# Performance work log

Measured on AMD Instinct MI355X. Metric: run time of the kernel, lower is better.

## Reference

```python
import jax, jax.numpy as jnp
import numpy as np

N_NODES = 50000
N_EDGES = 800000
IN_CH = 64
EDGE_DIM = 8
HIDDEN = 128
NUM_GRAPHS = 256


def setup_inputs() -> dict:
    key = jax.random.key(0)
    ks = jax.random.split(key, 16)
    x = jax.random.normal(ks[0], (N_NODES, IN_CH), dtype=jnp.float32)
    edge_index = jax.random.randint(ks[1], (2, N_EDGES), 0, N_NODES, dtype=jnp.int64)
    edge_attr = jax.random.normal(ks[2], (N_EDGES, EDGE_DIM), dtype=jnp.float32)
    batch = jnp.sort(jax.random.randint(ks[3], (N_NODES,), 0, NUM_GRAPHS, dtype=jnp.int64))

    def lin(k, fan_in, fan_out):
        bound = 1.0 / np.sqrt(fan_in)
        kw, kb = jax.random.split(k)
        W = jax.random.uniform(kw, (fan_in, fan_out), minval=-bound, maxval=bound, dtype=jnp.float32)
        b = jax.random.uniform(kb, (fan_out,), minval=-bound, maxval=bound, dtype=jnp.float32)
        return W, b

    W1, b1 = lin(ks[4], IN_CH, HIDDEN)
    We1, be1 = lin(ks[5], EDGE_DIM, IN_CH)
    W2, b2 = lin(ks[6], HIDDEN, HIDDEN)
    We2, be2 = lin(ks[7], EDGE_DIM, HIDDEN)
    W3, b3 = lin(ks[8], HIDDEN, HIDDEN)
    We3, be3 = lin(ks[9], EDGE_DIM, HIDDEN)
    return {"x": x, "edge_index": edge_index, "edge_attr": edge_attr, "batch": batch,
            "W1": W1, "b1": b1, "We1": We1, "be1": be1,
            "W2": W2, "b2": b2, "We2": We2, "be2": be2,
            "W3": W3, "b3": b3, "We3": We3, "be3": be3}


def gine_conv(x, src, dst, edge_attr, W, b, We, be):
    # edge feature projection to node-feature dim, then message = relu(x_j + e)
    e = edge_attr @ We + be                      # [E, d]
    msg = jax.nn.relu(x[src] + e)                # [E, d]
    agg = jax.ops.segment_sum(msg, dst, num_segments=x.shape[0])  # [N, d]
    # eps = 0 (PyG default, not trainable)
    return (x + agg) @ W + b


def reference(x, edge_index, edge_attr, batch,
              W1, b1, We1, be1, W2, b2, We2, be2, W3, b3, We3, be3):
    x = x.astype(jnp.float32)
    edge_attr = edge_attr.astype(jnp.float32)
    src, dst = edge_index[0], edge_index[1]
    x = jax.nn.relu(gine_conv(x, src, dst, edge_attr, W1, b1, We1, be1))
    x = jax.nn.relu(gine_conv(x, src, dst, edge_attr, W2, b2, We2, be2))
    x = jax.nn.relu(gine_conv(x, src, dst, edge_attr, W3, b3, We3, be3))
    # global mean pool over graphs
    sums = jax.ops.segment_sum(x, batch, num_segments=NUM_GRAPHS)          # [G, d]
    counts = jax.ops.segment_sum(jnp.ones((x.shape[0],), x.dtype), batch, num_segments=NUM_GRAPHS)
    return sums / jnp.maximum(counts, 1.0)[:, None]
```

## Files before the change

### kernel.cpp

```cpp
#include <hip/hip_runtime.h>
#include <hip/hip_bf16.h>
#include <hip/hip_fp16.h>

#define N_NODES 50000
#define N_EDGES 800000
#define IN_CH 64
#define EDGE_DIM 8
#define HIDDEN 128
#define NUM_GRAPHS 256
#define NPASS 2
#define PASS_W ((N_NODES + NPASS - 1) / NPASS)

typedef __attribute__((ext_vector_type(8))) _Float16 half8;
typedef __attribute__((ext_vector_type(4))) float floatx4;
typedef __attribute__((ext_vector_type(4))) int intx4;

static __device__ __forceinline__ __half2 u2h(int u) {
    union { int i; __half2 h; } cv; cv.i = u; return cv.h;
}
static __device__ __forceinline__ int h2u(__half2 h) {
    union { __half2 h; int i; } cv; cv.h = h; return cv.i;
}
static __device__ __forceinline__ unsigned short h1u(__half h) {
    union { __half h; unsigned short u; } cv; cv.h = h; return cv.u;
}

__global__ __launch_bounds__(256) void hist_kernel(
    const int* __restrict__ dst, int* __restrict__ deg, int E)
{
    int i = blockIdx.x * blockDim.x + threadIdx.x;
    if (i < E) atomicAdd(&deg[dst[i]], 1);
}

__global__ __launch_bounds__(256) void scan1_kernel(
    const int* __restrict__ deg, int* __restrict__ incl,
    int* __restrict__ blockSums, int N)
{
    __shared__ int s[256];
    int b = blockIdx.x, t = threadIdx.x;
    int i0 = b * 512 + 2 * t;
    int a0 = (i0 < N) ? deg[i0] : 0;
    int a1 = (i0 + 1 < N) ? deg[i0 + 1] : 0;
    int ps = a0 + a1;
    s[t] = ps;
    __syncthreads();
    for (int off = 1; off < 256; off <<= 1) {
        int v = (t >= off) ? s[t - off] : 0;
        __syncthreads();
        s[t] += v;
        __syncthreads();
    }
    int exclp = s[t] - ps;
    if (i0 < N)     incl[i0]     = exclp + a0;
    if (i0 + 1 < N) incl[i0 + 1] = exclp + a0 + a1;
    if (t == 255) blockSums[b] = s[255];
}

__global__ __launch_bounds__(128) void scan2_kernel(int* __restrict__ blockSums, int B)
{
    __shared__ int s[128];
    int t = threadIdx.x;
    int v = (t < B) ? blockSums[t] : 0;
    s[t] = v;
    __syncthreads();
    for (int off = 1; off < 128; off <<= 1) {
        int u = (t >= off) ? s[t - off] : 0;
        __syncthreads();
        s[t] += u;
        __syncthreads();
    }
    if (t < B) blockSums[t] = s[t] - v;
}

__global__ __launch_bounds__(256) void scan3_kernel(
    const int* __restrict__ incl, const int* __restrict__ deg,
    const int* __restrict__ blockSums, int* __restrict__ rowptr,
    int* __restrict__ pos, int N)
{
    int i = blockIdx.x * blockDim.x + threadIdx.x;
    if (i >= N) return;
    int v = incl[i] - deg[i] + blockSums[i >> 9];
    rowptr[i] = v;
    pos[i] = v;
}

__global__ __launch_bounds__(256) void scatter_pass_kernel(
    const int* __restrict__ dst, int* __restrict__ pos,
    int* __restrict__ eid, int lo, int E)
{
    int e = blockIdx.x * blockDim.x + threadIdx.x;
    if (e >= E) return;
    int d = dst[e];
    if ((unsigned)(d - lo) >= (unsigned)PASS_W) return;
    int p = atomicAdd(&pos[d], 1);
    eid[p] = e;
}

__global__ __launch_bounds__(256) void ranksort_gather_kernel(
    const int* __restrict__ eid, const int* __restrict__ src,
    const float* __restrict__ ea,
    const int* __restrict__ rowptr, const int* __restrict__ deg,
    int* __restrict__ src_s, __half* __restrict__ ea16, int N)
{
    int wave = threadIdx.x >> 6;
    int lane = threadIdx.x & 63;
    int n = blockIdx.x * 4 + wave;
    if (n >= N) return;
    int s = __builtin_amdgcn_readfirstlane(rowptr[n]);
    int d = __builtin_amdgcn_readfirstlane(deg[n]);

    if (d <= 64) {
        int e = (lane < d) ? eid[s + lane] : 0x7fffffff;
        int rank = 0;
        for (int i = 0; i < d; ++i) {
            int v = __builtin_amdgcn_readlane(e, i);
            rank += (v < e) ? 1 : 0;
        }
        if (lane < d) {
            int p = s + rank;
            src_s[p] = src[e];
            const float4* q = (const float4*)(ea + (size_t)e * EDGE_DIM);
            float4 a = q[0], b = q[1];
            __half2* o = (__half2*)(ea16 + (size_t)p * EDGE_DIM);
            o[0] = __floats2half2_rn(a.x, a.y);
            o[1] = __floats2half2_rn(a.z, a.w);
            o[2] = __floats2half2_rn(b.x, b.y);
            o[3] = __floats2half2_rn(b.z, b.w);
        }
    } else {
        for (int l = lane; l < d; l += 64) {
            int e = eid[s + l];
            int rank = 0;
            for (int i = 0; i < d; ++i)
                rank += (eid[s + i] < e) ? 1 : 0;
            int p = s + rank;
            src_s[p] = src[e];
            const float4* q = (const float4*)(ea + (size_t)e * EDGE_DIM);
            float4 a = q[0], b = q[1];
            __half2* o = (__half2*)(ea16 + (size_t)p * EDGE_DIM);
            o[0] = __floats2half2_rn(a.x, a.y);
            o[1] = __floats2half2_rn(a.z, a.w);
            o[2] = __floats2half2_rn(b.x, b.y);
            o[3] = __floats2half2_rn(b.z, b.w);
        }
    }
}

#define XH_ELEMS (N_NODES * IN_CH)
__global__ __launch_bounds__(256) void cvt_all_kernel(
    const float* __restrict__ x, __half* __restrict__ xh,
    const float* __restrict__ W1, const float* __restrict__ W2,
    const float* __restrict__ W3,
    _Float16* __restrict__ Wt1, _Float16* __restrict__ Wt2,
    _Float16* __restrict__ Wt3)
{
    int idx = blockIdx.x * blockDim.x + threadIdx.x;
    if (idx < XH_ELEMS) { xh[idx] = __float2half(x[idx]); return; }
    idx -= XH_ELEMS;
    if (idx < 128 * IN_CH) {
        int n = idx / IN_CH, k = idx - n * IN_CH;
        Wt1[idx] = (_Float16)W1[k * 128 + n];
        return;
    }
    idx -= 128 * IN_CH;
    if (idx < 128 * HIDDEN) {
        int n = idx / HIDDEN, k = idx - n * HIDDEN;
        Wt2[idx] = (_Float16)W2[k * 128 + n];
        return;
    }
    idx -= 128 * HIDDEN;
    if (idx < 128 * HIDDEN) {
        int n = idx / HIDDEN, k = idx - n * HIDDEN;
        Wt3[idx] = (_Float16)W3[k * 128 + n];
    }
}

#define BF 8

__global__ __launch_bounds__(256) void gather_xs128_kernel(
    const __half* __restrict__ h,
    const int*    __restrict__ src_s,
    const __half* __restrict__ ea16,
    const int*    __restrict__ rowptr,
    const int*    __restrict__ deg,
    const float*  __restrict__ We,
    const float*  __restrict__ be,
    __half*       __restrict__ xs,
    int N)
{
    int wave = threadIdx.x >> 6;
    int n    = blockIdx.x * 4 + wave;
    if (n >= N) return;
    int l  = threadIdx.x & 63;
    int j0 = 2 * l;

    __half2 hw[8];
    #pragma unroll
    for (int k = 0; k < 8; ++k) {
        float2 wv = *(const float2*)&We[k * 128 + j0];
        hw[k] = __floats2half2_rn(wv.x, wv.y);
    }
    float2 bevf = *(const float2*)&be[j0];
    __half2 bev2 = __floats2half2_rn(bevf.x, bevf.y);

    int start = __builtin_amdgcn_readfirstlane(rowptr[n]);
    int dg    = __builtin_amdgcn_readfirstlane(deg[n]);

    float2 hf = __half22float2(*(const __half2*)&h[(size_t)n * 128 + j0]);
    float acc0 = hf.x, acc1 = hf.y;

    int nb = dg / BF;
    int base = start;
    for (int b = 0; b < nb; ++b, base += BF) {
        int sid[BF];
        #pragma unroll
        for (int t = 0; t < BF; ++t)
            sid[t] = __builtin_amdgcn_readfirstlane(
                __builtin_nontemporal_load(&src_s[base + t]));
        __half2 hraw[BF];
        #pragma unroll
        for (int t = 0; t < BF; ++t)
            hraw[t] = *(const __half2*)&h[(size_t)sid[t] * 128 + j0];
        intx4 eav[BF];
        #pragma unroll
        for (int t = 0; t < BF; ++t)
            eav[t] = __builtin_nontemporal_load(
                (const intx4*)&ea16[(size_t)(base + t) * 8]);

        #pragma unroll
        for (int t = 0; t < BF; ++t) {
            __half2 e01 = u2h(eav[t].x), e23 = u2h(eav[t].y);
            __half2 e45 = u2h(eav[t].z), e67 = u2h(eav[t].w);
            __half2 m = __hfma2(__low2half2(e01),  hw[0], bev2);
            m = __hfma2(__high2half2(e01), hw[1], m);
            m = __hfma2(__low2half2(e23),  hw[2], m);
            m = __hfma2(__high2half2(e23), hw[3], m);
            m = __hfma2(__low2half2(e45),  hw[4], m);
            m = __hfma2(__high2half2(e45), hw[5], m);
            m = __hfma2(__low2half2(e67),  hw[6], m);
            m = __hfma2(__high2half2(e67), hw[7], m);
            m = __hadd2(m, hraw[t]);
            float2 mf = __half22float2(m);
            acc0 += mf.x > 0.0f ? mf.x : 0.0f;
            acc1 += mf.y > 0.0f ? mf.y : 0.0f;
        }
    }
    int end = start + dg;
    for (int idx = base; idx < end; ++idx) {
        int s = __builtin_amdgcn_readfirstlane(src_s[idx]);
        __half2 hr = *(const __half2*)&h[(size_t)s * 128 + j0];
        intx4 ev = __builtin_nontemporal_load((const intx4*)&ea16[(size_t)idx * 8]);
        __half2 e01 = u2h(ev.x), e23 = u2h(ev.y), e45 = u2h(ev.z), e67 = u2h(ev.w);
        __half2 m = __hfma2(__low2half2(e01),  hw[0], bev2);
        m = __hfma2(__high2half2(e01), hw[1], m);
        m = __hfma2(__low2half2(e23),  hw[2], m);
        m = __hfma2(__high2half2(e23), hw[3], m);
        m = __hfma2(__low2half2(e45),  hw[4], m);
        m = __hfma2(__high2half2(e45), hw[5], m);
        m = __hfma2(__low2half2(e67),  hw[6], m);
        m = __hfma2(__high2half2(e67), hw[7], m);
        m = __hadd2(m, hr);
        float2 mf = __half22float2(m);
        acc0 += mf.x > 0.0f ? mf.x : 0.0f;
        acc1 += mf.y > 0.0f ? mf.y : 0.0f;
    }
    __builtin_nontemporal_store(h2u(__floats2half2_rn(acc0, acc1)),
                                (int*)&xs[(size_t)n * 128 + j0]);
}

__global__ __launch_bounds__(256) void gather_xs64_kernel(
    const __half* __restrict__ h,
    const int*    __restrict__ src_s,
    const __half* __restrict__ ea16,
    const int*    __restrict__ rowptr,
    const int*    __restrict__ deg,
    const float*  __restrict__ We,
    const float*  __restrict__ be,
    __half*       __restrict__ xs,
    int N)
{
    int wave = threadIdx.x >> 6;
    int n    = blockIdx.x * 4 + wave;
    if (n >= N) return;
    int j = threadIdx.x & 63;

    __half2 w2[4];
    #pragma unroll
    for (int p = 0; p < 4; ++p)
        w2[p] = __floats2half2_rn(We[(2 * p) * 64 + j], We[(2 * p + 1) * 64 + j]);
    float bej = be[j];

    int start = __builtin_amdgcn_readfirstlane(rowptr[n]);
    int dg    = __builtin_amdgcn_readfirstlane(deg[n]);

    float acc = __half2float(h[(size_t)n * 64 + j]);

    int nb = dg / BF;
    int base = start;
    for (int b = 0; b < nb; ++b, base += BF) {
        int sid[BF];
        #pragma unroll
        for (int t = 0; t < BF; ++t)
            sid[t] = __builtin_amdgcn_readfirstlane(
                __builtin_nontemporal_load(&src_s[base + t]));
        __half hraw[BF];
        #pragma unroll
        for (int t = 0; t < BF; ++t)
            hraw[t] = h[(size_t)sid[t] * 64 + j];
        intx4 eav[BF];
        #pragma unroll
        for (int t = 0; t < BF; ++t)
            eav[t] = __builtin_nontemporal_load(
                (const intx4*)&ea16[(size_t)(base + t) * 8]);

        #pragma unroll
        for (int t = 0; t < BF; ++t) {
            __half2 d = __hmul2(u2h(eav[t].x), w2[0]);
            d = __hfma2(u2h(eav[t].y), w2[1], d);
            d = __hfma2(u2h(eav[t].z), w2[2], d);
            d = __hfma2(u2h(eav[t].w), w2[3], d);
            float proj = __half2float(__low2half(d)) + __half2float(__high2half(d));
            float m = __half2float(hraw[t]) + proj + bej;
            acc += m > 0.0f ? m : 0.0f;
        }
    }
    int end = start + dg;
    for (int idx = base; idx < end; ++idx) {
        int s = __builtin_amdgcn_readfirstlane(src_s[idx]);
        __half hr = h[(size_t)s * 64 + j];
        intx4 ev = __builtin_nontemporal_load((const intx4*)&ea16[(size_t)idx * 8]);
        __half2 d = __hmul2(u2h(ev.x), w2[0]);
        d = __hfma2(u2h(ev.y), w2[1], d);
        d = __hfma2(u2h(ev.z), w2[2], d);
        d = __hfma2(u2h(ev.w), w2[3], d);
        float proj = __half2float(__low2half(d)) + __half2float(__high2half(d));
        float m = __half2float(hr) + proj + bej;
        acc += m > 0.0f ? m : 0.0f;
    }
    __builtin_nontemporal_store(h1u(__float2half(acc)),
                                (unsigned short*)&xs[(size_t)n * 64 + j]);
}

template<int K>
__global__ __launch_bounds__(256) void node_mfma_kernel(
    const _Float16* __restrict__ xs,
    const _Float16* __restrict__ Wt,
    const float*    __restrict__ b,
    _Float16*       __restrict__ out,
    int N)
{
    int wave  = threadIdx.x >> 6;
    int lane  = threadIdx.x & 63;
    int row16 = lane & 15;
    int quad  = lane >> 4;
    int m0    = (blockIdx.x * 4 + wave) * 32;

    int nA = m0 + row16;        if (nA >= N) nA = N - 1;
    int nB = m0 + 16 + row16;   if (nB >= N) nB = N - 1;

    floatx4 accA[8], accB[8];
    #pragma unroll
    for (int t = 0; t < 8; ++t) { accA[t] = (floatx4)(0.0f); accB[t] = (floatx4)(0.0f); }

    #pragma unroll
    for (int kc = 0; kc < K; kc += 32) {
        half8 a0 = __builtin_nontemporal_load((const half8*)&xs[(size_t)nA * K + kc + quad * 8]);
        half8 a1 = __builtin_nontemporal_load((const half8*)&xs[(size_t)nB * K + kc + quad * 8]);
        #pragma unroll
        for (int t = 0; t < 8; ++t) {
            half8 bf = *(const half8*)&Wt[(size_t)(t * 16 + row16) * K + kc + quad * 8];
            accA[t] = __builtin_amdgcn_mfma_f32_16x16x32_f16(a0, bf, accA[t], 0, 0, 0);
            accB[t] = __builtin_amdgcn_mfma_f32_16x16x32_f16(a1, bf, accB[t], 0, 0, 0);
        }
    }

    #pragma unroll
    for (int t = 0; t < 8; ++t) {
        int col = t * 16 + row16;
        float bj = b[col];
        #pragma unroll
        for (int r = 0; r < 4; ++r) {
            int nodeA = m0 + quad * 4 + r;
            if (nodeA < N) {
                float v = accA[t][r] + bj;
                out[(size_t)nodeA * 128 + col] = (_Float16)(v > 0.0f ? v : 0.0f);
            }
            int nodeB = m0 + 16 + quad * 4 + r;
            if (nodeB < N) {
                float v = accB[t][r] + bj;
                out[(size_t)nodeB * 128 + col] = (_Float16)(v > 0.0f ? v : 0.0f);
            }
        }
    }
}

__global__ __launch_bounds__(256) void pool_kernel(
    const __half* __restrict__ h,
    const int*    __restrict__ batch,
    float*        __restrict__ out,
    int N)
{
    __shared__ int s_lo, s_hi;
    __shared__ float part[4][128];
    int g  = blockIdx.x;
    int t  = threadIdx.x;
    int fp = t & 63;
    int r  = t >> 6;

    if (t == 0) {
        int lo = 0, hi = N;
        while (lo < hi) { int m = (lo + hi) >> 1; if (batch[m] < g) lo = m + 1; else hi = m; }
        s_lo = lo;
        int lo2 = lo, hi2 = N;
        while (lo2 < hi2) { int m = (lo2 + hi2) >> 1; if (batch[m] < g + 1) lo2 = m + 1; else hi2 = m; }
        s_hi = lo2;
    }
    __syncthreads();

    int lo = s_lo, hi = s_hi;
    float a0 = 0.0f, a1 = 0.0f;
    for (int n = lo + r; n < hi; n += 4) {
        float2 f = __half22float2(*(const __half2*)&h[(size_t)n * 128 + 2 * fp]);
        a0 += f.x; a1 += f.y;
    }
    part[r][2 * fp]     = a0;
    part[r][2 * fp + 1] = a1;
    __syncthreads();

    if (r == 0) {
        float s0 = part[0][2 * fp] + part[1][2 * fp] + part[2][2 * fp] + part[3][2 * fp];
        float s1 = part[0][2 * fp + 1] + part[1][2 * fp + 1] + part[2][2 * fp + 1] + part[3][2 * fp + 1];
        float c = (float)(hi - lo);
        float d = c > 1.0f ? c : 1.0f;
        out[g * HIDDEN + 2 * fp]     = s0 / d;
        out[g * HIDDEN + 2 * fp + 1] = s1 / d;
    }
}

extern "C" void kernel_launch(void* const* d_in, const int* in_sizes, int n_in,
                              void* d_out, int out_size, void* d_ws, size_t ws_size,
                              hipStream_t stream)
{
    const float* x   = (const float*)d_in[0];
    const int*   ei  = (const int*)d_in[1];
    const float* ea  = (const float*)d_in[2];
    const int*   bat = (const int*)d_in[3];
    const float* W1  = (const float*)d_in[4];
    const float* b1  = (const float*)d_in[5];
    const float* We1 = (const float*)d_in[6];
    const float* be1 = (const float*)d_in[7];
    const float* W2  = (const float*)d_in[8];
    const float* b2  = (const float*)d_in[9];
    const float* We2 = (const float*)d_in[10];
    const float* be2 = (const float*)d_in[11];
    const float* W3  = (const float*)d_in[12];
    const float* b3  = (const float*)d_in[13];
    const float* We3 = (const float*)d_in[14];
    const float* be3 = (const float*)d_in[15];
    float* out = (float*)d_out;

    const int* src = ei;
    const int* dst = ei + N_EDGES;

    int* deg       = (int*)d_ws;
    int* rowptr    = deg + N_NODES;
    int* pos       = rowptr + N_NODES;
    int* eid       = pos + N_NODES;
    int* src_s     = eid + N_EDGES;
    int* blockSums = src_s + N_EDGES;
    __half* ea16   = (__half*)(blockSums + 128);
    __half* xs     = ea16 + (size_t)N_EDGES * EDGE_DIM;
    __half* xh     = xs + (size_t)N_NODES * HIDDEN;
    __half* h1h    = xh + (size_t)N_NODES * IN_CH;
    __half* h2h    = h1h + (size_t)N_NODES * HIDDEN;
    _Float16* Wt1  = (_Float16*)(h2h + (size_t)N_NODES * HIDDEN);
    _Float16* Wt2  = Wt1 + 128 * IN_CH;
    _Float16* Wt3  = Wt2 + 128 * HIDDEN;

    const int BLK = 256;
    const int NB_E = (N_EDGES + BLK - 1) / BLK;
    const int NB_N = (N_NODES + BLK - 1) / BLK;
    const int SCAN_B = (N_NODES + 511) / 512;
    const int MFMA_B = (N_NODES + 127) / 128;
    const int WAVE4_B = (N_NODES + 3) / 4;
    const int CVT_ELEMS = XH_ELEMS + 128 * IN_CH + 2 * 128 * HIDDEN;

    (void)hipMemsetAsync(deg, 0, N_NODES * sizeof(int), stream);
    hist_kernel<<<NB_E, BLK, 0, stream>>>(dst, deg, N_EDGES);
    scan1_kernel<<<SCAN_B, 256, 0, stream>>>(deg, pos, blockSums, N_NODES);
    scan2_kernel<<<1, 128, 0, stream>>>(blockSums, SCAN_B);
    scan3_kernel<<<NB_N, BLK, 0, stream>>>(pos, deg, blockSums, rowptr, pos, N_NODES);
    for (int pass = 0; pass < NPASS; ++pass) {
        scatter_pass_kernel<<<NB_E, BLK, 0, stream>>>(
            dst, pos, eid, pass * PASS_W, N_EDGES);
    }
    ranksort_gather_kernel<<<WAVE4_B, BLK, 0, stream>>>(
        eid, src, ea, rowptr, deg, src_s, ea16, N_NODES);
    cvt_all_kernel<<<(CVT_ELEMS + BLK - 1) / BLK, BLK, 0, stream>>>(
        x, xh, W1, W2, W3, Wt1, Wt2, Wt3);

    gather_xs64_kernel<<<WAVE4_B, BLK, 0, stream>>>(
        xh, src_s, ea16, rowptr, deg, We1, be1, xs, N_NODES);
    node_mfma_kernel<IN_CH><<<MFMA_B, 256, 0, stream>>>(
        (const _Float16*)xs, Wt1, b1, (_Float16*)h1h, N_NODES);

    gather_xs128_kernel<<<WAVE4_B, BLK, 0, stream>>>(
        h1h, src_s, ea16, rowptr, deg, We2, be2, xs, N_NODES);
    node_mfma_kernel<HIDDEN><<<MFMA_B, 256, 0, stream>>>(
        (const _Float16*)xs, Wt2, b2, (_Float16*)h2h, N_NODES);

    gather_xs128_kernel<<<WAVE4_B, BLK, 0, stream>>>(
        h2h, src_s, ea16, rowptr, deg, We3, be3, xs, N_NODES);
    node_mfma_kernel<HIDDEN><<<MFMA_B, 256, 0, stream>>>(
        (const _Float16*)xs, Wt3, b3, (_Float16*)h1h, N_NODES);

    pool_kernel<<<NUM_GRAPHS, 256, 0, stream>>>(h1h, bat, out, N_NODES);
}
```

Measured before the change: 426.0 us.

## Scatter edge records directly and use fixed-point accumulation for order-independent sums

Removes the rank-sort gather kernel by having the scatter passes write source ids and half-precision edge attributes directly at their atomic CSR slot. Because this makes within-node edge order nondeterministic, the gather kernels now accumulate messages as scaled integers so the sum no longer depends on order. The number of scatter passes is also raised. This trades an extra kernel and the eid round-trip for extra passes over the dst array and quantization error (truncation at 1/256) in aggregated messages.

```diff
diff --git a/kernel.cpp b/kernel.cpp
--- a/kernel.cpp
+++ b/kernel.cpp
@@ -8,8 +8,10 @@
 #define EDGE_DIM 8
 #define HIDDEN 128
 #define NUM_GRAPHS 256
-#define NPASS 2
+#define NPASS 4
 #define PASS_W ((N_NODES + NPASS - 1) / NPASS)
+#define QSCALE 256.0f
+#define QINV   (1.0f / 256.0f)
 
 typedef __attribute__((ext_vector_type(8))) _Float16 half8;
 typedef __attribute__((ext_vector_type(4))) float floatx4;
@@ -84,66 +86,25 @@
     pos[i] = v;
 }
 
-__global__ __launch_bounds__(256) void scatter_pass_kernel(
-    const int* __restrict__ dst, int* __restrict__ pos,
-    int* __restrict__ eid, int lo, int E)
+__global__ __launch_bounds__(256) void scatter_rec_kernel(
+    const int* __restrict__ dst, const int* __restrict__ src,
+    const float* __restrict__ ea, int* __restrict__ pos,
+    int* __restrict__ src_s, __half* __restrict__ ea16, int lo, int E)
 {
     int e = blockIdx.x * blockDim.x + threadIdx.x;
     if (e >= E) return;
     int d = dst[e];
     if ((unsigned)(d - lo) >= (unsigned)PASS_W) return;
     int p = atomicAdd(&pos[d], 1);
-    eid[p] = e;
-}
-
-__global__ __launch_bounds__(256) void ranksort_gather_kernel(
-    const int* __restrict__ eid, const int* __restrict__ src,
-    const float* __restrict__ ea,
-    const int* __restrict__ rowptr, const int* __restrict__ deg,
-    int* __restrict__ src_s, __half* __restrict__ ea16, int N)
-{
-    int wave = threadIdx.x >> 6;
-    int lane = threadIdx.x & 63;
-    int n = blockIdx.x * 4 + wave;
-    if (n >= N) return;
-    int s = __builtin_amdgcn_readfirstlane(rowptr[n]);
-    int d = __builtin_amdgcn_readfirstlane(deg[n]);
-
-    if (d <= 64) {
-        int e = (lane < d) ? eid[s + lane] : 0x7fffffff;
-        int rank = 0;
-        for (int i = 0; i < d; ++i) {
-            int v = __builtin_amdgcn_readlane(e, i);
-            rank += (v < e) ? 1 : 0;
-        }
-        if (lane < d) {
-            int p = s + rank;
-            src_s[p] = src[e];
-            const float4* q = (const float4*)(ea + (size_t)e * EDGE_DIM);
-            float4 a = q[0], b = q[1];
-            __half2* o = (__half2*)(ea16 + (size_t)p * EDGE_DIM);
-            o[0] = __floats2half2_rn(a.x, a.y);
-            o[1] = __floats2half2_rn(a.z, a.w);
-            o[2] = __floats2half2_rn(b.x, b.y);
-            o[3] = __floats2half2_rn(b.z, b.w);
-        }
-    } else {
-        for (int l = lane; l < d; l += 64) {
-            int e = eid[s + l];
-            int rank = 0;
-            for (int i = 0; i < d; ++i)
-                rank += (eid[s + i] < e) ? 1 : 0;
-            int p = s + rank;
-            src_s[p] = src[e];
-            const float4* q = (const float4*)(ea + (size_t)e * EDGE_DIM);
-            float4 a = q[0], b = q[1];
-            __half2* o = (__half2*)(ea16 + (size_t)p * EDGE_DIM);
-            o[0] = __floats2half2_rn(a.x, a.y);
-            o[1] = __floats2half2_rn(a.z, a.w);
-            o[2] = __floats2half2_rn(b.x, b.y);
-            o[3] = __floats2half2_rn(b.z, b.w);
-        }
-    }
+    __builtin_nontemporal_store(src[e], &src_s[p]);
+    const float4* q = (const float4*)(ea + (size_t)e * EDGE_DIM);
+    float4 a = q[0], b = q[1];
+    intx4 r;
+    r.x = h2u(__floats2half2_rn(a.x, a.y));
+    r.y = h2u(__floats2half2_rn(a.z, a.w));
+    r.z = h2u(__floats2half2_rn(b.x, b.y));
+    r.w = h2u(__floats2half2_rn(b.z, b.w));
+    __builtin_nontemporal_store(r, (intx4*)(ea16 + (size_t)p * EDGE_DIM));
 }
 
 #define XH_ELEMS (N_NODES * IN_CH)
@@ -207,7 +168,7 @@
     int dg    = __builtin_amdgcn_readfirstlane(deg[n]);
 
     float2 hf = __half22float2(*(const __half2*)&h[(size_t)n * 128 + j0]);
-    float acc0 = hf.x, acc1 = hf.y;
+    int acci0 = 0, acci1 = 0;
 
     int nb = dg / BF;
     int base = start;
@@ -241,8 +202,8 @@
             m = __hfma2(__high2half2(e67), hw[7], m);
             m = __hadd2(m, hraw[t]);
             float2 mf = __half22float2(m);
-            acc0 += mf.x > 0.0f ? mf.x : 0.0f;
-            acc1 += mf.y > 0.0f ? mf.y : 0.0f;
+            acci0 += (int)((mf.x > 0.0f ? mf.x : 0.0f) * QSCALE);
+            acci1 += (int)((mf.y > 0.0f ? mf.y : 0.0f) * QSCALE);
         }
     }
     int end = start + dg;
@@ -261,9 +222,11 @@
         m = __hfma2(__high2half2(e67), hw[7], m);
         m = __hadd2(m, hr);
         float2 mf = __half22float2(m);
-        acc0 += mf.x > 0.0f ? mf.x : 0.0f;
-        acc1 += mf.y > 0.0f ? mf.y : 0.0f;
-    }
+        acci0 += (int)((mf.x > 0.0f ? mf.x : 0.0f) * QSCALE);
+        acci1 += (int)((mf.y > 0.0f ? mf.y : 0.0f) * QSCALE);
+    }
+    float acc0 = hf.x + (float)acci0 * QINV;
+    float acc1 = hf.y + (float)acci1 * QINV;
     __builtin_nontemporal_store(h2u(__floats2half2_rn(acc0, acc1)),
                                 (int*)&xs[(size_t)n * 128 + j0]);
 }
@@ -293,7 +256,8 @@
     int start = __builtin_amdgcn_readfirstlane(rowptr[n]);
     int dg    = __builtin_amdgcn_readfirstlane(deg[n]);
 
-    float acc = __half2float(h[(size_t)n * 64 + j]);
+    float selff = __half2float(h[(size_t)n * 64 + j]);
+    int acci = 0;
 
     int nb = dg / BF;
     int base = start;
@@ -321,7 +285,7 @@
             d = __hfma2(u2h(eav[t].w), w2[3], d);
             float proj = __half2float(__low2half(d)) + __half2float(__high2half(d));
             float m = __half2float(hraw[t]) + proj + bej;
-            acc += m > 0.0f ? m : 0.0f;
+            acci += (int)((m > 0.0f ? m : 0.0f) * QSCALE);
         }
     }
     int end = start + dg;
@@ -335,8 +299,9 @@
         d = __hfma2(u2h(ev.w), w2[3], d);
         float proj = __half2float(__low2half(d)) + __half2float(__high2half(d));
         float m = __half2float(hr) + proj + bej;
-        acc += m > 0.0f ? m : 0.0f;
-    }
+        acci += (int)((m > 0.0f ? m : 0.0f) * QSCALE);
+    }
+    float acc = selff + (float)acci * QINV;
     __builtin_nontemporal_store(h1u(__float2half(acc)),
                                 (unsigned short*)&xs[(size_t)n * 64 + j]);
 }
@@ -476,6 +441,7 @@
     _Float16* Wt1  = (_Float16*)(h2h + (size_t)N_NODES * HIDDEN);
     _Float16* Wt2  = Wt1 + 128 * IN_CH;
     _Float16* Wt3  = Wt2 + 128 * HIDDEN;
+    (void)eid;
 
     const int BLK = 256;
     const int NB_E = (N_EDGES + BLK - 1) / BLK;
@@ -491,11 +457,9 @@
     scan2_kernel<<<1, 128, 0, stream>>>(blockSums, SCAN_B);
     scan3_kernel<<<NB_N, BLK, 0, stream>>>(pos, deg, blockSums, rowptr, pos, N_NODES);
     for (int pass = 0; pass < NPASS; ++pass) {
-        scatter_pass_kernel<<<NB_E, BLK, 0, stream>>>(
-            dst, pos, eid, pass * PASS_W, N_EDGES);
-    }
-    ranksort_gather_kernel<<<WAVE4_B, BLK, 0, stream>>>(
-        eid, src, ea, rowptr, deg, src_s, ea16, N_NODES);
+        scatter_rec_kernel<<<NB_E, BLK, 0, stream>>>(
+            dst, src, ea, pos, src_s, ea16, pass * PASS_W, N_EDGES);
+    }
     cvt_all_kernel<<<(CVT_ELEMS + BLK - 1) / BLK, BLK, 0, stream>>>(
         x, xh, W1, W2, W3, Wt1, Wt2, Wt3);
 
```

Result: slower. 436.8 us (+2.5%).
